# Kernel optimization log

Hardware: AMD Instinct MI355X
Metric: run time of the kernel (lower is better)

The kernel has to match this reference:

```python
import jax, jax.numpy as jnp
import numpy as np

VOCAB = 8000
IN_FEATURES = 256
P = 8  # half-window; neighbor_num = 2*P
B, L = 16, 2048


def setup_inputs() -> dict:
    key = jax.random.key(0)
    k1, k2, k3, k4 = jax.random.split(key, 4)
    input_ids = jax.random.randint(k1, (B, L), 0, VOCAB, dtype=jnp.int32)
    # node_embedding: default torch init (normal), padding_idx=0 row zeroed
    node_emb = jax.random.normal(k2, (VOCAB, IN_FEATURES), dtype=jnp.float32)
    node_emb = node_emb.at[0].set(0.0)
    # edge_weight and node_weight re-initialized with xavier_uniform (padding row NOT re-zeroed, matching source)
    lim_e = float(np.sqrt(6.0 / (VOCAB * VOCAB + 1 + 1)))
    edge_w = jax.random.uniform(k3, (VOCAB * VOCAB + 1, 1), minval=-lim_e, maxval=lim_e, dtype=jnp.float32)
    lim_n = float(np.sqrt(6.0 / (VOCAB + 1)))
    node_w = jax.random.uniform(k4, (VOCAB, 1), minval=-lim_n, maxval=lim_n, dtype=jnp.float32)
    return {"input_ids": input_ids, "node_emb": node_emb, "edge_w": edge_w, "node_w": node_w}


def _neighbors(input_ids):
    # vectorized sliding-window neighbor construction (replaces the python loop)
    b, l = input_ids.shape
    xp = jnp.pad(input_ids, ((0, 0), (P, P)))  # (B, L+2P)
    offsets = jnp.concatenate([jnp.arange(P), jnp.arange(P + 1, 2 * P + 1)])  # (2P,)
    idx = jnp.arange(l)[:, None] + offsets[None, :]  # (L, 2P)
    NX = xp[:, idx]  # (B, L, 2P)
    EW = input_ids[:, :, None].astype(jnp.int32) * VOCAB + NX
    EW = jnp.where(NX == 0, 0, EW)
    return NX, EW


def reference(input_ids, node_emb, edge_w, node_w):
    NX, EW = _neighbors(input_ids)
    Ra = node_emb[NX]              # (B, L, 2P, D) gather
    Ean = edge_w[EW]               # (B, L, 2P, 1) gather
    Mn = jnp.max(Ra * Ean, axis=2)  # (B, L, D) max over neighbors
    Rn = node_emb[input_ids]       # (B, L, D)
    Nn = node_w[input_ids]         # (B, L, 1)
    y = (1.0 - Nn) * Mn + Nn * Rn   # gated sum
    return y.sum(axis=1)           # (B, D)
```

## Files before the change

kernel.cpp:

```cpp
#include <hip/hip_runtime.h>


#define VOCAB 8000
#define FDIM  256
#define PNB   8
#define NK    16
#define BB    16
#define LL    2048
#define CHUNK 16
#define WIN   (CHUNK + 2*PNB)

__global__ void gnn_zero_out(float* __restrict__ out) {
    out[blockIdx.x * 256 + threadIdx.x] = 0.0f;
}

__global__ __launch_bounds__(256) void gnn_kernel(
    const int*   __restrict__ ids,
    const float* __restrict__ emb,
    const float* __restrict__ edge_w,
    const float* __restrict__ node_w,
    float*       __restrict__ out)
{
    __shared__ float s_emb[WIN][FDIM];
    __shared__ float s_ew [CHUNK][NK];
    __shared__ int   s_tok[WIN];
    __shared__ float s_nw [CHUNK];
    __shared__ float s_red[4][FDIM];

    const int b   = blockIdx.y;
    const int l0  = blockIdx.x * CHUNK;
    const int tid = threadIdx.x;
    const int* idrow = ids + b * LL;

    if (tid < WIN) {
        const int p = l0 - PNB + tid;
        int t = (p >= 0 && p < LL) ? idrow[p] : 0;
        t = (t < 0) ? 0 : ((t >= VOCAB) ? (VOCAB - 1) : t);
        s_tok[tid] = t;
    }
    __syncthreads();

    {
        const int ll = tid >> 4;
        const int k  = tid & (NK - 1);
        const int n  = s_tok[ll + k + (k >= PNB ? 1 : 0)];
        const int c  = s_tok[ll + PNB];
        const long long ei = (n == 0) ? 0LL : (long long)c * VOCAB + n;
        s_ew[ll][k] = edge_w[ei];
        if (tid < CHUNK) s_nw[tid] = node_w[s_tok[tid + PNB]];
    }
    {
        #pragma unroll
        for (int j = 0; j < 8; ++j) {
            const int i    = tid + 256 * j;
            const int row  = i >> 6;
            const int col4 = (i & 63) << 2;
            const float4 v = *(const float4*)(emb + (size_t)s_tok[row] * FDIM + col4);
            *(float4*)&s_emb[row][col4] = v;
        }
    }
    __syncthreads();

    const int wave = tid >> 6;
    const int lane = tid & 63;
    const int f0   = lane << 2;

    float4 acc = make_float4(0.f, 0.f, 0.f, 0.f);
    #pragma unroll
    for (int q = 0; q < CHUNK / 4; ++q) {
        const int ll = (wave << 2) + q;
        const float nw = s_nw[ll];
        float4 m = make_float4(-INFINITY, -INFINITY, -INFINITY, -INFINITY);
        #pragma unroll
        for (int k = 0; k < NK; ++k) {
            const int widx = ll + k + (k >= PNB ? 1 : 0);
            const float  e = s_ew[ll][k];
            const float4 r = *(const float4*)&s_emb[widx][f0];
            m.x = fmaxf(m.x, e * r.x);
            m.y = fmaxf(m.y, e * r.y);
            m.z = fmaxf(m.z, e * r.z);
            m.w = fmaxf(m.w, e * r.w);
        }
        const float4 rc = *(const float4*)&s_emb[ll + PNB][f0];
        const float w1 = 1.0f - nw;
        acc.x += w1 * m.x + nw * rc.x;
        acc.y += w1 * m.y + nw * rc.y;
        acc.z += w1 * m.z + nw * rc.z;
        acc.w += w1 * m.w + nw * rc.w;
    }

    ((float4*)s_red[wave])[lane] = acc;
    __syncthreads();

    const float s = s_red[0][tid] + s_red[1][tid] + s_red[2][tid] + s_red[3][tid];
    atomicAdd(out + b * FDIM + tid, s);
}

extern "C" void kernel_launch(void* const* d_in, const int* in_sizes, int n_in,
                              void* d_out, int out_size, void* d_ws, size_t ws_size,
                              hipStream_t stream) {
    const int*   ids    = nullptr;
    const float* emb    = nullptr;
    const float* edge_w = nullptr;
    const float* node_w = nullptr;
    for (int i = 0; i < n_in; ++i) {
        const long long sz = in_sizes[i];
        if      (sz == (long long)BB * LL)            ids    = (const int*)  d_in[i];
        else if (sz == (long long)VOCAB * FDIM)       emb    = (const float*)d_in[i];
        else if (sz == (long long)VOCAB * VOCAB + 1)  edge_w = (const float*)d_in[i];
        else if (sz == (long long)VOCAB)              node_w = (const float*)d_in[i];
    }
    float* out = (float*)d_out;

    gnn_zero_out<<<dim3(out_size / 256), dim3(256), 0, stream>>>(out);

    dim3 grid(LL / CHUNK, BB);
    gnn_kernel<<<grid, 256, 0, stream>>>(ids, emb, edge_w, node_w, out);
}
```

Measured before the change: 322.3 us.

## Reuse shared-memory embedding rows across four tokens and use nontemporal edge loads

The inner compute loop is restructured so each wave walks the 20-row sliding window once and applies each loaded embedding row to all four tokens whose neighborhoods contain it. This cuts LDS float4 reads from 68 to 20 per wave. The random edge-weight gathers are also made nontemporal so they do not pollute the cache. It costs more registers for four running maxima and four center rows.

```diff
diff --git a/kernel.cpp b/kernel.cpp
--- a/kernel.cpp
+++ b/kernel.cpp
@@ -46,7 +46,7 @@
         const int n  = s_tok[ll + k + (k >= PNB ? 1 : 0)];
         const int c  = s_tok[ll + PNB];
         const long long ei = (n == 0) ? 0LL : (long long)c * VOCAB + n;
-        s_ew[ll][k] = edge_w[ei];
+        s_ew[ll][k] = __builtin_nontemporal_load(edge_w + ei);
         if (tid < CHUNK) s_nw[tid] = node_w[s_tok[tid + PNB]];
     }
     {
@@ -64,29 +64,39 @@
     const int wave = tid >> 6;
     const int lane = tid & 63;
     const int f0   = lane << 2;
+    const int base = wave << 2;
+
+    float4 m[4], rc[4];
+    #pragma unroll
+    for (int q = 0; q < 4; ++q)
+        m[q] = make_float4(-INFINITY, -INFINITY, -INFINITY, -INFINITY);
+
+    #pragma unroll
+    for (int j = 0; j < 20; ++j) {
+        const float4 r = *(const float4*)&s_emb[base + j][f0];
+        #pragma unroll
+        for (int q = 0; q < 4; ++q) {
+            const int d = j - q;
+            if (d < 0 || d > 16) continue;
+            if (d == 8) { rc[q] = r; continue; }
+            const int   k = (d < 8) ? d : d - 1;
+            const float e = s_ew[base + q][k];
+            m[q].x = fmaxf(m[q].x, e * r.x);
+            m[q].y = fmaxf(m[q].y, e * r.y);
+            m[q].z = fmaxf(m[q].z, e * r.z);
+            m[q].w = fmaxf(m[q].w, e * r.w);
+        }
+    }
 
     float4 acc = make_float4(0.f, 0.f, 0.f, 0.f);
     #pragma unroll
-    for (int q = 0; q < CHUNK / 4; ++q) {
-        const int ll = (wave << 2) + q;
-        const float nw = s_nw[ll];
-        float4 m = make_float4(-INFINITY, -INFINITY, -INFINITY, -INFINITY);
-        #pragma unroll
-        for (int k = 0; k < NK; ++k) {
-            const int widx = ll + k + (k >= PNB ? 1 : 0);
-            const float  e = s_ew[ll][k];
-            const float4 r = *(const float4*)&s_emb[widx][f0];
-            m.x = fmaxf(m.x, e * r.x);
-            m.y = fmaxf(m.y, e * r.y);
-            m.z = fmaxf(m.z, e * r.z);
-            m.w = fmaxf(m.w, e * r.w);
-        }
-        const float4 rc = *(const float4*)&s_emb[ll + PNB][f0];
+    for (int q = 0; q < 4; ++q) {
+        const float nw = s_nw[base + q];
         const float w1 = 1.0f - nw;
-        acc.x += w1 * m.x + nw * rc.x;
-        acc.y += w1 * m.y + nw * rc.y;
-        acc.z += w1 * m.z + nw * rc.z;
-        acc.w += w1 * m.w + nw * rc.w;
+        acc.x += w1 * m[q].x + nw * rc[q].x;
+        acc.y += w1 * m[q].y + nw * rc[q].y;
+        acc.z += w1 * m[q].z + nw * rc[q].z;
+        acc.w += w1 * m[q].w + nw * rc[q].w;
     }
 
     ((float4*)s_red[wave])[lane] = acc;
```

Result: no change. 318.7 us (-1.1%).
